# Performance work log

Hardware: AMD Instinct MI355X
Metric: run time of the kernel (lower is better)

The kernel has to match this reference:

```python
import jax, jax.numpy as jnp
import numpy as np

N, R, K, B, M, D = 300000, 1200, 20, 256, 50, 100


def setup_inputs() -> dict:
    key = jax.random.key(0)
    ks = jax.random.split(key, 16)
    w = lambda k, s: jax.random.normal(k, s, dtype=jnp.float32) * 0.1
    return {
        "node_embedding": jax.random.normal(ks[0], (N, D), dtype=jnp.float32),
        "relation_embedding": jax.random.normal(ks[1], (R, D), dtype=jnp.float32),
        "origin_embedding": jax.random.normal(ks[2], (B, D), dtype=jnp.float32),
        "graph_embedding": jax.random.normal(ks[3], (B, D), dtype=jnp.float32),
        "actor_w1": w(ks[4], (3 * D, D)), "actor_b1": jnp.zeros((D,), jnp.float32),
        "actor_w2": w(ks[5], (D, D)), "actor_b2": jnp.zeros((D,), jnp.float32),
        "actor_w3": w(ks[6], (D, 1)), "actor_b3": jnp.zeros((1,), jnp.float32),
        "critic_w1": w(ks[7], (3 * D, D)), "critic_b1": jnp.zeros((D,), jnp.float32),
        "critic_w2": w(ks[8], (D, D)), "critic_b2": jnp.zeros((D,), jnp.float32),
        "critic_w3": w(ks[9], (D, 1)), "critic_b3": jnp.zeros((1,), jnp.float32),
        "entity_adj": jax.random.randint(ks[10], (N, K), 0, N, dtype=jnp.int64),
        "relation_adj": jax.random.randint(ks[11], (N, K), 0, R, dtype=jnp.int64),
        "nodes": jax.random.randint(ks[12], (B, M), 0, N, dtype=jnp.int64),
    }


def _head(x, w1, b1, w2, b2, w3, b3):
    # tanh(L1) -> tanh(L2) -> sigmoid(L3), per Net.forward
    h = jnp.tanh(x @ w1 + b1)
    h = jnp.tanh(h @ w2 + b2)
    return jax.nn.sigmoid(h @ w3 + b3)


def reference(node_embedding, relation_embedding, origin_embedding, graph_embedding,
              actor_w1, actor_b1, actor_w2, actor_b2, actor_w3, actor_b3,
              critic_w1, critic_b1, critic_w2, critic_b2, critic_w3, critic_b3,
              entity_adj, relation_adj, nodes):
    # one-hop KG expansion: gather neighbor entity / relation ids of frontier nodes
    neigh_ids = entity_adj[nodes]          # [B, M, K]
    rel_ids = relation_adj[nodes]          # [B, M, K]
    neigh = node_embedding[neigh_ids]      # [B, M, K, D]
    rel = relation_embedding[rel_ids]      # [B, M, K, D]
    action = jnp.concatenate([neigh, rel], axis=-1)                    # [B, M, K, 2D]
    state = jnp.broadcast_to(graph_embedding[:, None, None, :], neigh.shape)
    x = jnp.concatenate([state, action], axis=-1)                      # [B, M, K, 3D]
    act_probs = _head(x, actor_w1, actor_b1, actor_w2, actor_b2, actor_w3, actor_b3)
    q_actions = _head(x, critic_w1, critic_b1, critic_w2, critic_b2, critic_w3, critic_b3)
    # get_sim_reward_batch: dot_rewards + updated graph embedding
    b, m, k, d = neigh.shape
    flat_node = neigh.reshape(b, m * k, d)                             # [B, M*K, D]
    ge = graph_embedding[:, None, :]                                   # [B, 1, D]
    dot_rewards = jax.nn.softmax(
        jnp.sum(origin_embedding[:, None, :] * (ge + flat_node), axis=-1), axis=-1)
    new_graph_embedding = ge + flat_node                               # [B, M*K, D]
    return (act_probs, q_actions, dot_rewards, new_graph_embedding)
```

## Files before the change

### kernel.cpp

```cpp
#include <hip/hip_runtime.h>
#include <hip/hip_bf16.h>

#define NND 300000
#define RR 1200
#define KADJ 20
#define BB 256
#define MM 50
#define DD 100
#define ROWS (BB*MM*KADJ)
#define MKJ (MM*KADJ)
#define N1P 208
#define K1S 8
#define NT1 7
#define NT2 7
#define K2S 4
#define H1S 136

typedef __attribute__((ext_vector_type(8))) short short8;
typedef __attribute__((ext_vector_type(4))) float f32x4;

__device__ inline unsigned short f2bf(float f) {
  union { float f; unsigned u; } v; v.f = f;
  return (unsigned short)((v.u + 0x7FFFu + ((v.u >> 16) & 1u)) >> 16);
}
__device__ inline unsigned pkbf2(float x, float y) {
  __hip_bfloat162 p = __float22bfloat162_rn(make_float2(x, y));
  unsigned u; __builtin_memcpy(&u, &p, 4); return u;
}
__device__ inline float fast_tanh(float x) {
  float e = __builtin_amdgcn_exp2f(x * 2.885390082f);
  float r = __builtin_amdgcn_rcpf(e + 1.f);
  return __builtin_fmaf(-2.f, r, 1.f);
}
__device__ inline float fast_sigmoid(float x) {
  float e = __builtin_amdgcn_exp2f(x * -1.442695041f);
  return __builtin_amdgcn_rcpf(1.f + e);
}

__global__ __launch_bounds__(256) void k_prep(
    const float* __restrict__ gemb,
    const float* __restrict__ aw1, const float* __restrict__ ab1,
    const float* __restrict__ cw1, const float* __restrict__ cb1,
    const float* __restrict__ aw2, const float* __restrict__ cw2,
    short* __restrict__ wf1, short* __restrict__ wf2, float* __restrict__ G1) {
  int t = blockIdx.x * blockDim.x + threadIdx.x;
  if (t < 57344) {
    int j = t & 7, l = (t >> 3) & 63, f = t >> 9;
    int ks = f & 7, r2 = f >> 3;
    int nt = r2 % 7, h = r2 / 7;
    int kp = ks * 32 + ((l >> 4) * 8) + j;
    int n = nt * 16 + (l & 15);
    float v = 0.f;
    if (n < DD) {
      const float* w1 = h ? cw1 : aw1;
      if (kp < DD) v = w1[(DD + kp) * DD + n];
      else if (kp >= 128 && kp < 228) v = w1[(200 + kp - 128) * DD + n];
    }
    wf1[t] = (short)f2bf(v);
    return;
  }
  int t2 = t - 57344;
  if (t2 < 28672) {
    int j = t2 & 7, l = (t2 >> 3) & 63, f = t2 >> 9;
    int ks = f & 3, r2 = f >> 2;
    int nt = r2 % 7, h = r2 / 7;
    int k = ks * 32 + ((l >> 4) * 8) + j;
    int n = nt * 16 + (l & 15);
    float v = 0.f;
    if (k < DD && n < DD) v = (h ? cw2 : aw2)[k * DD + n];
    wf2[t2] = (short)f2bf(v);
    return;
  }
  int t3 = t2 - 28672;
  if (t3 < BB * N1P) {
    int b = t3 / N1P, n = t3 % N1P;
    float acc = 0.f;
    if (n < 200) {
      const float* w1 = (n < DD) ? aw1 : cw1;
      const float* b1 = (n < DD) ? ab1 : cb1;
      int jj = (n < DD) ? n : n - DD;
      acc = b1[jj];
      for (int d = 0; d < DD; ++d) acc += gemb[b * DD + d] * w1[d * DD + jj];
    }
    G1[t3] = acc;
  }
}

__global__ __launch_bounds__(256) void k_soft(float* __restrict__ dr) {
  __shared__ float red[4];
  int b = blockIdx.x, tid = threadIdx.x;
  int lane = tid & 63, w = tid >> 6;
  float* p = dr + (size_t)b * MKJ;
  float v[4], mx = -1e30f;
  #pragma unroll
  for (int i = 0; i < 4; ++i) {
    int j = tid + i * 256;
    v[i] = (j < MKJ) ? p[j] : -1e30f;
    mx = fmaxf(mx, v[i]);
  }
  #pragma unroll
  for (int off = 32; off; off >>= 1) mx = fmaxf(mx, __shfl_xor(mx, off, 64));
  if (lane == 0) red[w] = mx;
  __syncthreads();
  mx = fmaxf(fmaxf(red[0], red[1]), fmaxf(red[2], red[3]));
  float e[4], se = 0.f;
  #pragma unroll
  for (int i = 0; i < 4; ++i) {
    e[i] = __expf(v[i] - mx);
    if (tid + i * 256 < MKJ) se += e[i];
  }
  #pragma unroll
  for (int off = 32; off; off >>= 1) se += __shfl_xor(se, off, 64);
  __syncthreads();
  if (lane == 0) red[w] = se;
  __syncthreads();
  se = red[0] + red[1] + red[2] + red[3];
  float inv = 1.f / se;
  #pragma unroll
  for (int i = 0; i < 4; ++i) {
    int j = tid + i * 256;
    if (j < MKJ) p[j] = e[i] * inv;
  }
}

template<bool FUSE>
__global__ __launch_bounds__(256, 4) void k_all(
    const float* __restrict__ nemb, const float* __restrict__ remb,
    const float* __restrict__ oemb, const float* __restrict__ gemb,
    const int* __restrict__ eadj, const int* __restrict__ radj,
    const int* __restrict__ nodes,
    const short* __restrict__ wf1, const short* __restrict__ wf2,
    const float* __restrict__ G1,
    const float* __restrict__ ab2, const float* __restrict__ cb2,
    const float* __restrict__ aw3, const float* __restrict__ ab3,
    const float* __restrict__ cw3, const float* __restrict__ cb3,
    float* __restrict__ outA, float* __restrict__ outQ,
    float* __restrict__ dots, float* __restrict__ outNG) {
  __shared__ uint4 WB[2][512];
  __shared__ unsigned short H1[64 * H1S];
  __shared__ float G1s[224], b2s[224], w3s[224];
  __shared__ float gs[128], os[128];
  __shared__ int nidS[64], ridS[64];

  int hid = blockIdx.x;
  int x = hid & 15, b = hid >> 4;
  int tid = threadIdx.x;
  int lane = tid & 63, w = tid >> 6, ln = lane & 15, lg = lane >> 4;

  if (tid < 64) {
    int row = x * 64 + tid;
    int rc = row < MKJ ? row : MKJ - 1;
    int m = rc / KADJ, kk = rc - m * KADJ;
    int v = nodes[b * MM + m];
    nidS[tid] = eadj[v * KADJ + kk];
    ridS[tid] = radj[v * KADJ + kk];
  }
  for (int i = tid; i < 224; i += 256) {
    int h = i / 112, n = i - h * 112;
    G1s[i] = (n < DD) ? G1[b * N1P + h * DD + n] : 0.f;
    b2s[i] = (n < DD) ? (h ? cb2[n] : ab2[n]) : 0.f;
    w3s[i] = (n < DD) ? (h ? cw3[n] : aw3[n]) : 0.f;
  }
  if (FUSE) {
    for (int i = tid; i < 128; i += 256) {
      gs[i] = (i < DD) ? gemb[b * DD + i] : 0.f;
      os[i] = (i < DD) ? oemb[b * DD + i] : 0.f;
    }
  }
  __syncthreads();

  short8 a1[8];
  int myrow = w * 16 + ln;
  {
    const float* nrow = nemb + (size_t)nidS[myrow] * DD;
    const float* rrow = remb + (size_t)ridS[myrow] * DD;
    #pragma unroll
    for (int ks = 0; ks < 8; ++ks) {
      const float* src = (ks < 4) ? nrow : rrow;
      int cb = (ks & 3) * 32 + lg * 8;
      float4 lo = make_float4(0.f,0.f,0.f,0.f), hi = lo;
      if (cb <= 96) lo = *(const float4*)(src + cb);
      if (cb + 4 <= 96) hi = *(const float4*)(src + cb + 4);
      union { short8 s; unsigned u[4]; } fr;
      fr.u[0] = pkbf2(lo.x, lo.y); fr.u[1] = pkbf2(lo.z, lo.w);
      fr.u[2] = pkbf2(hi.x, hi.y); fr.u[3] = pkbf2(hi.z, hi.w);
      a1[ks] = fr.s;
    }
  }

  if (FUSE) {
    int grow = x * 64 + myrow;
    bool vrow = grow < MKJ;
    float* ngr = outNG + ((size_t)b * MKJ + grow) * DD;
    float pp = 0.f;
    #pragma unroll
    for (int ks = 0; ks < 4; ++ks) {
      int cb = ks * 32 + lg * 8;
      union { short8 s; unsigned short us[8]; } fr; fr.s = a1[ks];
      float t[8];
      #pragma unroll
      for (int q = 0; q < 8; ++q) {
        unsigned u = (unsigned)fr.us[q] << 16;
        float v; __builtin_memcpy(&v, &u, 4);
        t[q] = v + gs[cb + q];
        pp += os[cb + q] * t[q];
      }
      if (vrow && cb <= 96) {
        f32x4 t0; t0[0]=t[0]; t0[1]=t[1]; t0[2]=t[2]; t0[3]=t[3];
        __builtin_nontemporal_store(t0, (f32x4*)(ngr + cb));
        if (cb < 96) {
          f32x4 t1; t1[0]=t[4]; t1[1]=t[5]; t1[2]=t[6]; t1[3]=t[7];
          __builtin_nontemporal_store(t1, (f32x4*)(ngr + cb + 4));
        }
      }
    }
    pp += __shfl_xor(pp, 16, 64);
    pp += __shfl_xor(pp, 32, 64);
    if (lg == 0 && vrow) dots[(size_t)b * MKJ + grow] = pp;
  }

  float b3v[2] = {ab3[0], cb3[0]};
  float* outs[2] = {outA, outQ};

  for (int h = 0; h < 2; ++h) {
    const char* wf1b = (const char*)wf1 + (size_t)h * 57344;
    {
      const uint4* src = (const uint4*)wf1b;
      WB[0][tid * 2] = src[tid * 2];
      WB[0][tid * 2 + 1] = src[tid * 2 + 1];
    }
    int cur = 0;
    __syncthreads();
    for (int nt = 0; nt < NT1; ++nt) {
      uint4 s0, s1;
      if (nt < NT1 - 1) {
        const uint4* src = (const uint4*)(wf1b + (size_t)(nt + 1) * 8192);
        s0 = src[tid * 2];
        s1 = src[tid * 2 + 1];
      }
      int n = nt * 16 + ln;
      float g = G1s[h * 112 + n];
      f32x4 acc = {g, g, g, g};
      #pragma unroll
      for (int ks = 0; ks < K1S; ++ks) {
        short8 bw = *(const short8*)&WB[cur][ks * 64 + lane];
        acc = __builtin_amdgcn_mfma_f32_16x16x32_bf16(a1[ks], bw, acc, 0, 0, 0);
      }
      if (n < DD) {
        #pragma unroll
        for (int r = 0; r < 4; ++r)
          H1[(w * 16 + lg * 4 + r) * H1S + n] = f2bf(fast_tanh(acc[r]));
      }
      if (nt < NT1 - 1) {
        WB[cur ^ 1][tid * 2] = s0;
        WB[cur ^ 1][tid * 2 + 1] = s1;
        cur ^= 1;
      }
      __syncthreads();
    }

    short8 a2[4];
    #pragma unroll
    for (int ks = 0; ks < K2S; ++ks)
      a2[ks] = *(const short8*)&H1[myrow * H1S + ks * 32 + lg * 8];
    {
      union { short8 s; unsigned short us[8]; } m; m.s = a2[3];
      int cb = 96 + lg * 8;
      #pragma unroll
      for (int q = 0; q < 8; ++q) if (cb + q >= DD) m.us[q] = 0;
      a2[3] = m.s;
    }

    const char* wf2b = (const char*)wf2 + (size_t)h * 28672;
    WB[0][tid] = ((const uint4*)wf2b)[tid];
    cur = 0;
    __syncthreads();
    float part[4] = {0.f, 0.f, 0.f, 0.f};
    for (int nt = 0; nt < NT2; ++nt) {
      uint4 s0;
      if (nt < NT2 - 1)
        s0 = ((const uint4*)(wf2b + (size_t)(nt + 1) * 4096))[tid];
      f32x4 acc = {0.f, 0.f, 0.f, 0.f};
      #pragma unroll
      for (int ks = 0; ks < K2S; ++ks) {
        short8 bw = *(const short8*)&WB[cur][ks * 64 + lane];
        acc = __builtin_amdgcn_mfma_f32_16x16x32_bf16(a2[ks], bw, acc, 0, 0, 0);
      }
      int n = nt * 16 + ln;
      float b2v = b2s[h * 112 + n];
      float w3v = w3s[h * 112 + n];
      #pragma unroll
      for (int r = 0; r < 4; ++r)
        part[r] += fast_tanh(acc[r] + b2v) * w3v;
      if (nt < NT2 - 1) {
        WB[cur ^ 1][tid] = s0;
        cur ^= 1;
      }
      __syncthreads();
    }
    #pragma unroll
    for (int r = 0; r < 4; ++r) {
      float s = part[r];
      s += __shfl_xor(s, 1, 64); s += __shfl_xor(s, 2, 64);
      s += __shfl_xor(s, 4, 64); s += __shfl_xor(s, 8, 64);
      if (ln == 0) {
        int row = x * 64 + w * 16 + lg * 4 + r;
        if (row < MKJ) outs[h][(size_t)b * MKJ + row] = fast_sigmoid(s + b3v[h]);
      }
    }
    __syncthreads();
  }
}

__global__ __launch_bounds__(1024) void k_rewards(
    const float* __restrict__ nemb, const float* __restrict__ oemb,
    const float* __restrict__ gemb,
    const int* __restrict__ eadj, const int* __restrict__ nodes,
    float* __restrict__ outDR, float* __restrict__ outNG) {
  __shared__ float dots[MKJ];
  __shared__ float red[16];
  int b = blockIdx.x;
  int tid = threadIdx.x;
  int lane = tid & 63, w = tid >> 6;
  int d1 = lane + 64;
  float o0 = oemb[b * DD + lane];
  float g0 = gemb[b * DD + lane];
  float o1 = (d1 < DD) ? oemb[b * DD + d1] : 0.f;
  float g1 = (d1 < DD) ? gemb[b * DD + d1] : 0.f;
  for (int j = w; j < MKJ; j += 16) {
    int m = j / KADJ, kk = j - m * KADJ;
    int v = nodes[b * MM + m];
    int nid = eadj[v * KADJ + kk];
    const float* nr = nemb + (size_t)nid * DD;
    float s0 = g0 + nr[lane];
    float s1 = (d1 < DD) ? (g1 + nr[d1]) : 0.f;
    float* ngr = outNG + ((long long)b * MKJ + j) * DD;
    ngr[lane] = s0;
    if (d1 < DD) ngr[d1] = s1;
    float p = o0 * s0 + o1 * s1;
    p += __shfl_xor(p, 1, 64); p += __shfl_xor(p, 2, 64); p += __shfl_xor(p, 4, 64);
    p += __shfl_xor(p, 8, 64); p += __shfl_xor(p, 16, 64); p += __shfl_xor(p, 32, 64);
    if (lane == 0) dots[j] = p;
  }
  __syncthreads();
  float mx = -1e30f;
  for (int j = tid; j < MKJ; j += 1024) mx = fmaxf(mx, dots[j]);
  for (int off = 32; off; off >>= 1) mx = fmaxf(mx, __shfl_xor(mx, off, 64));
  if (lane == 0) red[w] = mx;
  __syncthreads();
  mx = red[0];
  #pragma unroll
  for (int i = 1; i < 16; ++i) mx = fmaxf(mx, red[i]);
  float se = 0.f;
  for (int j = tid; j < MKJ; j += 1024) se += __expf(dots[j] - mx);
  for (int off = 32; off; off >>= 1) se += __shfl_xor(se, off, 64);
  __syncthreads();
  if (lane == 0) red[w] = se;
  __syncthreads();
  se = 0.f;
  #pragma unroll
  for (int i = 0; i < 16; ++i) se += red[i];
  float inv = 1.f / se;
  for (int j = tid; j < MKJ; j += 1024) outDR[b * MKJ + j] = __expf(dots[j] - mx) * inv;
}

extern "C" void kernel_launch(void* const* d_in, const int* in_sizes, int n_in,
                              void* d_out, int out_size, void* d_ws, size_t ws_size,
                              hipStream_t stream) {
  const float* nemb = (const float*)d_in[0];
  const float* remb = (const float*)d_in[1];
  const float* oemb = (const float*)d_in[2];
  const float* gemb = (const float*)d_in[3];
  const float* aw1 = (const float*)d_in[4];
  const float* ab1 = (const float*)d_in[5];
  const float* aw2 = (const float*)d_in[6];
  const float* ab2 = (const float*)d_in[7];
  const float* aw3 = (const float*)d_in[8];
  const float* ab3 = (const float*)d_in[9];
  const float* cw1 = (const float*)d_in[10];
  const float* cb1 = (const float*)d_in[11];
  const float* cw2 = (const float*)d_in[12];
  const float* cb2 = (const float*)d_in[13];
  const float* cw3 = (const float*)d_in[14];
  const float* cb3 = (const float*)d_in[15];
  const int* eadj = (const int*)d_in[16];
  const int* radj = (const int*)d_in[17];
  const int* nodes = (const int*)d_in[18];

  float* out = (float*)d_out;
  float* outA = out;
  float* outQ = out + ROWS;
  float* outDR = out + 2 * ROWS;
  float* outNG = out + 3 * ROWS;

  const size_t need = 385024;
  bool fuse = ws_size >= need;
  char* scratch = (char*)d_ws;
  if (!fuse) {
    scratch = (char*)(out + ((size_t)3 * ROWS + (size_t)ROWS * DD - need / 4));
  }
  short* wf1 = (short*)scratch;
  short* wf2 = (short*)(scratch + 114688);
  float* G1 = (float*)(scratch + 172032);

  k_prep<<<544, 256, 0, stream>>>(gemb, aw1, ab1, cw1, cb1, aw2, cw2, wf1, wf2, G1);
  if (fuse) {
    k_all<true><<<4096, 256, 0, stream>>>(nemb, remb, oemb, gemb, eadj, radj, nodes,
                                          wf1, wf2, G1, ab2, cb2, aw3, ab3, cw3, cb3,
                                          outA, outQ, outDR, outNG);
    k_soft<<<BB, 256, 0, stream>>>(outDR);
  } else {
    k_all<false><<<4096, 256, 0, stream>>>(nemb, remb, oemb, gemb, eadj, radj, nodes,
                                           wf1, wf2, G1, ab2, cb2, aw3, ab3, cw3, cb3,
                                           outA, outQ, outDR, outNG);
    k_rewards<<<BB, 1024, 0, stream>>>(nemb, oemb, gemb, eadj, nodes, outDR, outNG);
  }
}
```

Measured before the change: 122.2 us.

## Coalesce new_graph_embedding stores via LDS staging and compute dots from fp32 gathers

The new_graph_embedding output is now written through a swizzled LDS staging buffer (reusing H1), so each thread writes contiguous float4 chunks across whole rows instead of strided per-row fragments. The dot-reward partial sums are computed from the fp32 gathered values inside the gather loop rather than from bf16-unpacked registers. Weight tile copies into LDS switch from tid*2 to tid/tid+256 indexing to coalesce global loads. This adds a __syncthreads and LDS traffic. The stored embedding still comes from bf16-rounded values, so its precision is unchanged.

```diff
diff --git a/kernel.cpp b/kernel.cpp
--- a/kernel.cpp
+++ b/kernel.cpp
@@ -171,6 +171,9 @@
 
   short8 a1[8];
   int myrow = w * 16 + ln;
+  int grow = x * 64 + myrow;
+  bool vrow = grow < MKJ;
+  float pp = 0.f;
   {
     const float* nrow = nemb + (size_t)nidS[myrow] * DD;
     const float* rrow = remb + (size_t)ridS[myrow] * DD;
@@ -185,38 +188,46 @@
       fr.u[0] = pkbf2(lo.x, lo.y); fr.u[1] = pkbf2(lo.z, lo.w);
       fr.u[2] = pkbf2(hi.x, hi.y); fr.u[3] = pkbf2(hi.z, hi.w);
       a1[ks] = fr.s;
+      if (FUSE && ks < 4 && cb <= 96) {
+        pp += os[cb+0]*(lo.x+gs[cb+0]) + os[cb+1]*(lo.y+gs[cb+1]) +
+              os[cb+2]*(lo.z+gs[cb+2]) + os[cb+3]*(lo.w+gs[cb+3]);
+        if (cb + 4 <= 96)
+          pp += os[cb+4]*(hi.x+gs[cb+4]) + os[cb+5]*(hi.y+gs[cb+5]) +
+                os[cb+6]*(hi.z+gs[cb+6]) + os[cb+7]*(hi.w+gs[cb+7]);
+      }
     }
   }
 
   if (FUSE) {
-    int grow = x * 64 + myrow;
-    bool vrow = grow < MKJ;
-    float* ngr = outNG + ((size_t)b * MKJ + grow) * DD;
-    float pp = 0.f;
-    #pragma unroll
-    for (int ks = 0; ks < 4; ++ks) {
-      int cb = ks * 32 + lg * 8;
-      union { short8 s; unsigned short us[8]; } fr; fr.s = a1[ks];
-      float t[8];
-      #pragma unroll
-      for (int q = 0; q < 8; ++q) {
-        unsigned u = (unsigned)fr.us[q] << 16;
-        float v; __builtin_memcpy(&v, &u, 4);
-        t[q] = v + gs[cb + q];
-        pp += os[cb + q] * t[q];
-      }
-      if (vrow && cb <= 96) {
-        f32x4 t0; t0[0]=t[0]; t0[1]=t[1]; t0[2]=t[2]; t0[3]=t[3];
-        __builtin_nontemporal_store(t0, (f32x4*)(ngr + cb));
-        if (cb < 96) {
-          f32x4 t1; t1[0]=t[4]; t1[1]=t[5]; t1[2]=t[6]; t1[3]=t[7];
-          __builtin_nontemporal_store(t1, (f32x4*)(ngr + cb + 4));
-        }
-      }
-    }
     pp += __shfl_xor(pp, 16, 64);
     pp += __shfl_xor(pp, 32, 64);
     if (lg == 0 && vrow) dots[(size_t)b * MKJ + grow] = pp;
+
+    #pragma unroll
+    for (int ks = 0; ks < 4; ++ks) {
+      int col = (ks * 32 + lg * 8) ^ ((myrow & 7) << 3);
+      *(short8*)&H1[myrow * H1S + col] = a1[ks];
+    }
+    __syncthreads();
+
+    const size_t ngbase = ((size_t)b * MKJ + (size_t)x * 64) * DD;
+    for (int q = tid; q < 1600; q += 256) {
+      int fidx = q * 4;
+      int row = fidx / DD;
+      int col = fidx - row * DD;
+      if (x * 64 + row < MKJ) {
+        int sc = ((col & ~7) ^ ((row & 7) << 3)) + (col & 7);
+        unsigned long long d = *(const unsigned long long*)&H1[row * H1S + sc];
+        f32x4 t;
+        #pragma unroll
+        for (int e = 0; e < 4; ++e) {
+          unsigned u = (unsigned)((d >> (16 * e)) & 0xFFFFull) << 16;
+          float v; __builtin_memcpy(&v, &u, 4);
+          t[e] = v + gs[col + e];
+        }
+        __builtin_nontemporal_store(t, (f32x4*)(outNG + ngbase + fidx));
+      }
+    }
   }
 
   float b3v[2] = {ab3[0], cb3[0]};
@@ -226,8 +237,8 @@
     const char* wf1b = (const char*)wf1 + (size_t)h * 57344;
     {
       const uint4* src = (const uint4*)wf1b;
-      WB[0][tid * 2] = src[tid * 2];
-      WB[0][tid * 2 + 1] = src[tid * 2 + 1];
+      WB[0][tid] = src[tid];
+      WB[0][tid + 256] = src[tid + 256];
     }
     int cur = 0;
     __syncthreads();
@@ -235,8 +246,8 @@
       uint4 s0, s1;
       if (nt < NT1 - 1) {
         const uint4* src = (const uint4*)(wf1b + (size_t)(nt + 1) * 8192);
-        s0 = src[tid * 2];
-        s1 = src[tid * 2 + 1];
+        s0 = src[tid];
+        s1 = src[tid + 256];
       }
       int n = nt * 16 + ln;
       float g = G1s[h * 112 + n];
@@ -252,8 +263,8 @@
           H1[(w * 16 + lg * 4 + r) * H1S + n] = f2bf(fast_tanh(acc[r]));
       }
       if (nt < NT1 - 1) {
-        WB[cur ^ 1][tid * 2] = s0;
-        WB[cur ^ 1][tid * 2 + 1] = s1;
+        WB[cur ^ 1][tid] = s0;
+        WB[cur ^ 1][tid + 256] = s1;
         cur ^= 1;
       }
       __syncthreads();
```

Result: faster. 111.0 us (-9.1%).
